# Optimization experiments

Measured on AMD Instinct MI355X. Metric: run time of the kernel, lower is better.

Reference implementation:

```python
import jax, jax.numpy as jnp
import numpy as np

N, P, E, IN = 50000, 4, 500000, 128   # nodes, metapaths, edges/metapath, in_size
H, F = 8, 32                           # num_heads, out_feats per head (hidden_size)
HF = H * F                             # flattened embedding (256)
HS = 128                               # semantic attention hidden size
B, OUT = 128, 2                        # num contracts (graphs), classes
NEG_SLOPE = 0.2                        # DGL GATConv LeakyReLU slope


def setup_inputs() -> dict:
    key = jax.random.key(0)
    ks = jax.random.split(key, 14)
    return {
        "h": jax.random.normal(ks[0], (N, IN), jnp.float32),
        "Wg": jax.random.normal(ks[1], (P, IN, HF), jnp.float32) * 0.1,
        "attn_l": jax.random.normal(ks[2], (P, H, F), jnp.float32) * 0.1,
        "attn_r": jax.random.normal(ks[3], (P, H, F), jnp.float32) * 0.1,
        "gat_bias": jax.random.normal(ks[4], (P, HF), jnp.float32) * 0.1,
        "sem_W1": jax.random.normal(ks[5], (HF, HS), jnp.float32) * 0.1,
        "sem_b1": jax.random.normal(ks[6], (HS,), jnp.float32) * 0.1,
        "sem_W2": jax.random.normal(ks[7], (HS, 1), jnp.float32) * 0.1,
        "cls_W": jax.random.normal(ks[8], (HF, OUT), jnp.float32) * 0.1,
        "cls_b": jax.random.normal(ks[9], (OUT,), jnp.float32) * 0.1,
        "src": jax.random.randint(ks[10], (P, E), 0, N, jnp.int32),
        "dst": jax.random.randint(ks[11], (P, E), 0, N, jnp.int32),
        "graph_ids": jax.random.randint(ks[12], (N,), 0, B, jnp.int32),
    }


def _gat(h, W, al, ar, bias, s, d):
    """One DGL-style GATConv over an edge list (dropout=identity, eval mode)."""
    n = h.shape[0]
    hp = (h @ W).reshape(n, H, F)                 # [N,H,F] projected features
    el = (hp * al).sum(-1)                        # [N,H] src attention term
    er = (hp * ar).sum(-1)                        # [N,H] dst attention term
    e = jax.nn.leaky_relu(el[s] + er[d], NEG_SLOPE)        # [E,H] edge scores
    m = jax.ops.segment_max(e, d, num_segments=n)          # per-dst max (softmax stab.)
    a = jnp.exp(e - m[d])                                  # [E,H]
    den = jax.ops.segment_sum(a, d, num_segments=n)        # [N,H]
    alpha = a / den[d]                                     # edge softmax over in-neighbors
    out = jax.ops.segment_sum(alpha[:, :, None] * hp[s], d, num_segments=n)  # [N,H,F]
    return jax.nn.elu(out + bias.reshape(1, H, F)).reshape(n, HF)


def reference(h, Wg, attn_l, attn_r, gat_bias, sem_W1, sem_b1, sem_W2,
              cls_W, cls_b, src, dst, graph_ids):
    n = h.shape[0]
    # GATConv per meta-path (small fixed loop over P=4 metapaths)
    embs = [_gat(h, Wg[p], attn_l[p], attn_r[p], gat_bias[p], src[p], dst[p])
            for p in range(Wg.shape[0])]
    z = jnp.stack(embs, axis=1)                   # [N,P,HF]
    # Semantic attention over meta-paths
    w = jnp.tanh(z @ sem_W1 + sem_b1) @ sem_W2    # [N,P,1]
    beta = jax.nn.softmax(w.mean(0), axis=0)      # [P,1]
    fused = (beta[None] * z).sum(1)               # [N,HF]
    # Per-graph (filename) mean pooling
    seg = jax.ops.segment_sum(fused, graph_ids, num_segments=B)
    cnt = jax.ops.segment_sum(jnp.ones((n,), fused.dtype), graph_ids, num_segments=B)
    pooled = seg / jnp.maximum(cnt, 1.0)[:, None]  # [B,HF]
    logits = pooled @ cls_W + cls_b                # [B,OUT]
    return (logits, pooled)
```

## Files before the change

### kernel.cpp

```cpp
#include <hip/hip_runtime.h>

#define NN 50000
#define PM 4
#define EE 500000
#define INF_ 128
#define NH 8
#define FF 32
#define HF 256
#define HS 128
#define BG 128
#define OUTC 2

#define NB2 98
#define BCAP 6144
#define BCH 4096
#define NBB 123
#define NGB 13
#define GCAP 576
#define NBG1 782
#define NBE 196
#define NBG2 782

typedef __attribute__((ext_vector_type(8))) short bf16x8;
typedef __attribute__((ext_vector_type(4))) float f32x4;

__device__ __forceinline__ float b2f(unsigned short x) {
  unsigned u = ((unsigned)x) << 16;
  return __builtin_bit_cast(float, u);
}
__device__ __forceinline__ unsigned short f2b(float f) {
  unsigned u = __builtin_bit_cast(unsigned, f);
  u += 0x7fff + ((u >> 16) & 1);
  return (unsigned short)(u >> 16);
}
__device__ __forceinline__ float fexp(float x) { return __expf(x); }
__device__ __forceinline__ float ftanh(float x) {
  float t = __expf(-2.f * fabsf(x));
  float r = (1.f - t) / (1.f + t);
  return copysignf(r, x);
}

__global__ __launch_bounds__(256) void prep_kernel(
    const float* __restrict__ h, const float* __restrict__ Wg,
    const float* __restrict__ W1, const float* __restrict__ al,
    const float* __restrict__ ar,
    unsigned short* __restrict__ h_b, unsigned short* __restrict__ Wb_t,
    unsigned short* __restrict__ W1_t, float* __restrict__ wl,
    float* __restrict__ wr, int* __restrict__ gcnt, int* __restrict__ gcnt2) {
  int b = blockIdx.x;
  int tid = threadIdx.x;
  if (b < 1) {
    for (int i = tid; i < PM * NB2; i += 256) gcnt[i] = 0;
    if (tid < BG) gcnt2[tid] = 0;
    return;
  }
  b -= 1;
  if (b < 6250) {
    int t = b * 256 + tid;
    float4 v = *(const float4*)(h + (size_t)t * 4);
    ushort4 o;
    o.x = f2b(v.x); o.y = f2b(v.y); o.z = f2b(v.z); o.w = f2b(v.w);
    *(ushort4*)(h_b + (size_t)t * 4) = o;
    return;
  }
  b -= 6250;
  if (b < 512) {
    int t = b * 256 + tid;
    int p = t >> 15, rem = t & 32767;
    int n = rem >> 7, k = rem & 127;
    Wb_t[(size_t)p * 32768 + n * 128 + k] = f2b(Wg[(size_t)p * 32768 + k * 256 + n]);
    return;
  }
  b -= 512;
  if (b < 128) {
    int t = b * 256 + tid;
    int n = t >> 8, k = t & 255;
    W1_t[n * 256 + k] = f2b(W1[k * 128 + n]);
    return;
  }
  b -= 128;
  {
    int t = b * 256 + tid;
    int p = t >> 10, rem = t & 1023;
    int k = rem >> 3, hh = rem & 7;
    const float* wrow = Wg + (size_t)p * 32768 + k * 256 + hh * 32;
    const float* alp = al + p * 256 + hh * 32;
    const float* arp = ar + p * 256 + hh * 32;
    float sl = 0.f, sr = 0.f;
    #pragma unroll
    for (int f = 0; f < 32; f++) { sl += wrow[f] * alp[f]; sr += wrow[f] * arp[f]; }
    wl[t] = sl; wr[t] = sr;
  }
}

__global__ __launch_bounds__(256) void bg_kernel(
    const int* __restrict__ src, const int* __restrict__ dst,
    unsigned* __restrict__ bdata, int* __restrict__ gcnt,
    const int* __restrict__ gid, int* __restrict__ glist,
    int* __restrict__ gcnt2) {
  __shared__ __align__(16) char smem[18432];
  int b = blockIdx.x;
  int tid = threadIdx.x;
  if (b < NBB * PM) {
    unsigned* ed = (unsigned*)smem;
    int* hist  = (int*)(smem + BCH * 4);
    int* gbase = hist + NB2;
    int* cur   = gbase + NB2;
    int p = b / NBB, blk = b % NBB;
    int e0 = blk * BCH;
    int n = min(BCH, EE - e0);
    if (tid < NB2) hist[tid] = 0;
    __syncthreads();
    const int* sp = src + (size_t)p * EE + e0;
    const int* dp = dst + (size_t)p * EE + e0;
    for (int i = tid; i < n; i += 256) {
      int s = sp[i], d = dp[i];
      ed[i] = ((unsigned)d << 16) | (unsigned)s;
      atomicAdd(&hist[d >> 9], 1);
    }
    __syncthreads();
    if (tid < NB2) {
      gbase[tid] = atomicAdd(&gcnt[p * NB2 + tid], hist[tid]);
      cur[tid] = 0;
    }
    __syncthreads();
    for (int i = tid; i < n; i += 256) {
      unsigned pk = ed[i];
      int bk = pk >> 25;
      int slot = gbase[bk] + atomicAdd(&cur[bk], 1);
      if (slot < BCAP)
        bdata[((size_t)(p * NB2 + bk)) * BCAP + slot] = pk;
    }
  } else {
    int* gl    = (int*)smem;
    int* hist  = (int*)(smem + BCH * 4);
    int* gbase = hist + BG;
    int* cur   = gbase + BG;
    int blk = b - NBB * PM;
    int e0 = blk * BCH;
    int n = min(BCH, NN - e0);
    if (tid < BG) hist[tid] = 0;
    __syncthreads();
    for (int i = tid; i < n; i += 256) {
      int g = gid[e0 + i];
      gl[i] = g;
      atomicAdd(&hist[g], 1);
    }
    __syncthreads();
    if (tid < BG) {
      gbase[tid] = atomicAdd(&gcnt2[tid], hist[tid]);
      cur[tid] = 0;
    }
    __syncthreads();
    for (int i = tid; i < n; i += 256) {
      int g = gl[i];
      int slot = gbase[g] + atomicAdd(&cur[g], 1);
      if (slot < GCAP) glist[g * GCAP + slot] = e0 + i;
    }
  }
}

__global__ __launch_bounds__(256) void csrify_kernel(
    const unsigned* __restrict__ bdata, const int* __restrict__ gcnt,
    int* __restrict__ off, unsigned short* __restrict__ csr) {
  __shared__ unsigned ebuf[BCAP];
  __shared__ int gc[NB2];
  __shared__ int degc[512];
  __shared__ int loff[513];
  __shared__ int tmp[256];
  __shared__ int base_s;
  int b = blockIdx.x, p = blockIdx.y;
  int tid = threadIdx.x;
  if (tid < NB2) gc[tid] = min(gcnt[p * NB2 + tid], BCAP);
  __syncthreads();
  if (tid == 0) {
    int s = 0;
    for (int i = 0; i < b; i++) s += gc[i];
    base_s = s;
  }
  int cnt = gc[b];
  const unsigned* bp = bdata + ((size_t)(p * NB2 + b)) * BCAP;
  for (int i = tid; i < cnt; i += 256) ebuf[i] = bp[i];
  degc[tid] = 0; degc[256 + tid] = 0;
  __syncthreads();
  for (int i = tid; i < cnt; i += 256)
    atomicAdd(&degc[(ebuf[i] >> 16) & 511], 1);
  __syncthreads();
  int d0 = degc[2 * tid], d1 = degc[2 * tid + 1];
  tmp[tid] = d0 + d1;
  __syncthreads();
  for (int o = 1; o < 256; o <<= 1) {
    int v = (tid >= o) ? tmp[tid - o] : 0;
    __syncthreads();
    tmp[tid] += v;
    __syncthreads();
  }
  int bse = tmp[tid] - d0 - d1;
  loff[2 * tid] = bse; loff[2 * tid + 1] = bse + d0;
  if (tid == 255) loff[512] = tmp[255];
  __syncthreads();
  int base = base_s;
  for (int dl = tid; dl < 512; dl += 256) {
    int n = b * 512 + dl;
    if (n <= NN) off[(size_t)p * (NN + 1) + n] = base + loff[dl];
  }
  degc[tid] = 0; degc[256 + tid] = 0;
  __syncthreads();
  for (int i = tid; i < cnt; i += 256) {
    unsigned pk = ebuf[i];
    int dl = (pk >> 16) & 511;
    int slot = loff[dl] + atomicAdd(&degc[dl], 1);
    csr[(size_t)p * EE + base + slot] = (unsigned short)(pk & 0xffff);
  }
}

__global__ __launch_bounds__(256) void g1elr_kernel(
    const unsigned short* __restrict__ hA, const unsigned short* __restrict__ Bt,
    unsigned short* __restrict__ Cb, const float* __restrict__ wl,
    const float* __restrict__ wr, float* __restrict__ el, float* __restrict__ er,
    int M, int p0, int npaths, size_t cstride, size_t estride) {
  __shared__ __align__(16) char smem[49152];
  int b = blockIdx.x;
  int tid = threadIdx.x;
  int nb1 = NBG1 * 2;
  if (b < nb1) {
    unsigned short* As = (unsigned short*)smem;
    unsigned short* Bs = (unsigned short*)(smem + 16384);
    int row0 = (b >> 1) * 64, col0 = (b & 1) * 128;
    #pragma unroll
    for (int i = 0; i < 4; i++) {
      int c = i * 256 + tid;
      int row = c >> 4, g = c & 15;
      int grow = row0 + row;
      uint4 v = make_uint4(0, 0, 0, 0);
      if (grow < M) v = *(const uint4*)(hA + (size_t)grow * 128 + g * 8);
      *(uint4*)&As[row * 128 + ((g ^ (row & 15)) << 3)] = v;
    }
    int wave = tid >> 6, lane = tid & 63;
    int ln = lane & 15, quad = lane >> 4;
    int mbase = (wave >> 1) * 32, nbase = (wave & 1) * 64;
    bf16x8 afr[4][2];
    bool afr_ok = false;
    for (int pl = 0; pl < npaths; pl++) {
      const unsigned short* Bp = Bt + (size_t)(p0 + pl) * 32768;
      #pragma unroll
      for (int i = 0; i < 8; i++) {
        int c = i * 256 + tid;
        int row = c >> 4, g = c & 15;
        uint4 v = *(const uint4*)(Bp + (size_t)(col0 + row) * 128 + g * 8);
        *(uint4*)&Bs[row * 128 + ((g ^ (row & 15)) << 3)] = v;
      }
      __syncthreads();
      if (!afr_ok) {
        #pragma unroll
        for (int ks = 0; ks < 4; ks++) {
          int g = ks * 4 + quad;
          #pragma unroll
          for (int mi = 0; mi < 2; mi++) {
            int r = mbase + mi * 16 + ln;
            afr[ks][mi] = *(const bf16x8*)&As[r * 128 + ((g ^ ln) << 3)];
          }
        }
        afr_ok = true;
      }
      f32x4 acc[2][4] = {};
      #pragma unroll
      for (int ks = 0; ks < 4; ks++) {
        int g = ks * 4 + quad;
        bf16x8 bb[4];
        #pragma unroll
        for (int ni = 0; ni < 4; ni++) {
          int r = nbase + ni * 16 + ln;
          bb[ni] = *(const bf16x8*)&Bs[r * 128 + ((g ^ ln) << 3)];
        }
        #pragma unroll
        for (int mi = 0; mi < 2; mi++)
          #pragma unroll
          for (int ni = 0; ni < 4; ni++)
            acc[mi][ni] = __builtin_amdgcn_mfma_f32_16x16x32_bf16(afr[ks][mi], bb[ni], acc[mi][ni], 0, 0, 0);
      }
      unsigned short* Cp = Cb + (size_t)pl * cstride;
      #pragma unroll
      for (int mi = 0; mi < 2; mi++) {
        int gm0 = row0 + mbase + mi * 16 + quad * 4;
        #pragma unroll
        for (int ni = 0; ni < 4; ni++) {
          int gn = col0 + nbase + ni * 16 + ln;
          #pragma unroll
          for (int r = 0; r < 4; r++) {
            int gm = gm0 + r;
            if (gm < M) Cp[(size_t)gm * 256 + gn] = f2b(acc[mi][ni][r]);
          }
        }
      }
      __syncthreads();
    }
  } else {
    float* wls = (float*)smem;
    float* wrs = wls + 1024;
    int t = b - nb1;
    int pl = t / NBE, nblk = t % NBE;
    const float* wlp = wl + (size_t)(p0 + pl) * 1024;
    const float* wrp = wr + (size_t)(p0 + pl) * 1024;
    float* elp = el + (size_t)pl * estride;
    float* erp = er + (size_t)pl * estride;
    for (int i = tid; i < 1024; i += 256) { wls[i] = wlp[i]; wrs[i] = wrp[i]; }
    __syncthreads();
    int n = nblk * 256 + tid;
    if (n >= M) return;
    float accl[8] = {}, accr[8] = {};
    for (int kk = 0; kk < 16; kk++) {
      uint4 raw = *(const uint4*)(hA + (size_t)n * 128 + kk * 8);
      unsigned uu[4] = {raw.x, raw.y, raw.z, raw.w};
      #pragma unroll
      for (int q = 0; q < 4; q++) {
        float v0 = __builtin_bit_cast(float, uu[q] << 16);
        float v1 = __builtin_bit_cast(float, uu[q] & 0xffff0000u);
        int k = kk * 8 + q * 2;
        #pragma unroll
        for (int hh = 0; hh < 8; hh++) {
          accl[hh] += v0 * wls[k * 8 + hh] + v1 * wls[(k + 1) * 8 + hh];
          accr[hh] += v0 * wrs[k * 8 + hh] + v1 * wrs[(k + 1) * 8 + hh];
        }
      }
    }
    *(float4*)(elp + (size_t)n * 8)     = make_float4(accl[0], accl[1], accl[2], accl[3]);
    *(float4*)(elp + (size_t)n * 8 + 4) = make_float4(accl[4], accl[5], accl[6], accl[7]);
    *(float4*)(erp + (size_t)n * 8)     = make_float4(accr[0], accr[1], accr[2], accr[3]);
    *(float4*)(erp + (size_t)n * 8 + 4) = make_float4(accr[4], accr[5], accr[6], accr[7]);
  }
}

__global__ __launch_bounds__(256) void agg_kernel(
    const unsigned short* __restrict__ hp_b, const float* __restrict__ el,
    const float* __restrict__ er, const unsigned short* __restrict__ csr,
    const int* __restrict__ off, const float* __restrict__ bias,
    unsigned short* __restrict__ emb_b, int N, int p0,
    size_t hstride, size_t estride, size_t embstride) {
  int pl = blockIdx.y;
  int p = p0 + pl;
  const unsigned short* hp = hp_b + (size_t)pl * hstride;
  const float* elp = el + (size_t)pl * estride;
  const float* erp = er + (size_t)pl * estride;
  const unsigned short* csrp = csr + (size_t)p * EE;
  const int* offp = off + (size_t)p * (NN + 1);
  const float* bp = bias + (size_t)p * HF;
  unsigned short* embp = emb_b + (size_t)pl * embstride;
  int n = blockIdx.x * 4 + (threadIdx.x >> 6);
  if (n >= N) return;
  int lane = threadIdx.x & 63;
  int h = lane >> 3;
  int e0 = offp[n], e1 = offp[n + 1];
  float erh = erp[n * NH + h];
  float den = 0.f, a0 = 0.f, a1 = 0.f, a2 = 0.f, a3 = 0.f;
  int e = e0;
  for (; e + 8 <= e1; e += 8) {
    int s[8];
    #pragma unroll
    for (int j = 0; j < 8; j++) s[j] = csrp[e + j];
    float x[8];
    #pragma unroll
    for (int j = 0; j < 8; j++) x[j] = elp[s[j] * NH + h];
    ushort4 hv[8];
    #pragma unroll
    for (int j = 0; j < 8; j++)
      hv[j] = *(const ushort4*)(hp + (size_t)s[j] * HF + lane * 4);
    float w[8];
    #pragma unroll
    for (int j = 0; j < 8; j++) {
      float xx = x[j] + erh;
      xx = fmaxf(xx, 0.2f * xx);
      w[j] = fexp(xx);
    }
    den += ((w[0] + w[1]) + (w[2] + w[3])) + ((w[4] + w[5]) + (w[6] + w[7]));
    a0 += ((w[0] * b2f(hv[0].x) + w[1] * b2f(hv[1].x)) + (w[2] * b2f(hv[2].x) + w[3] * b2f(hv[3].x)))
        + ((w[4] * b2f(hv[4].x) + w[5] * b2f(hv[5].x)) + (w[6] * b2f(hv[6].x) + w[7] * b2f(hv[7].x)));
    a1 += ((w[0] * b2f(hv[0].y) + w[1] * b2f(hv[1].y)) + (w[2] * b2f(hv[2].y) + w[3] * b2f(hv[3].y)))
        + ((w[4] * b2f(hv[4].y) + w[5] * b2f(hv[5].y)) + (w[6] * b2f(hv[6].y) + w[7] * b2f(hv[7].y)));
    a2 += ((w[0] * b2f(hv[0].z) + w[1] * b2f(hv[1].z)) + (w[2] * b2f(hv[2].z) + w[3] * b2f(hv[3].z)))
        + ((w[4] * b2f(hv[4].z) + w[5] * b2f(hv[5].z)) + (w[6] * b2f(hv[6].z) + w[7] * b2f(hv[7].z)));
    a3 += ((w[0] * b2f(hv[0].w) + w[1] * b2f(hv[1].w)) + (w[2] * b2f(hv[2].w) + w[3] * b2f(hv[3].w)))
        + ((w[4] * b2f(hv[4].w) + w[5] * b2f(hv[5].w)) + (w[6] * b2f(hv[6].w) + w[7] * b2f(hv[7].w)));
  }
  if (e + 4 <= e1) {
    int s0 = csrp[e], s1 = csrp[e + 1], s2 = csrp[e + 2], s3 = csrp[e + 3];
    float x0 = elp[s0 * NH + h] + erh;
    float x1 = elp[s1 * NH + h] + erh;
    float x2 = elp[s2 * NH + h] + erh;
    float x3 = elp[s3 * NH + h] + erh;
    ushort4 h0 = *(const ushort4*)(hp + (size_t)s0 * HF + lane * 4);
    ushort4 h1 = *(const ushort4*)(hp + (size_t)s1 * HF + lane * 4);
    ushort4 h2 = *(const ushort4*)(hp + (size_t)s2 * HF + lane * 4);
    ushort4 h3 = *(const ushort4*)(hp + (size_t)s3 * HF + lane * 4);
    x0 = fmaxf(x0, 0.2f * x0); x1 = fmaxf(x1, 0.2f * x1);
    x2 = fmaxf(x2, 0.2f * x2); x3 = fmaxf(x3, 0.2f * x3);
    float w0 = fexp(x0), w1 = fexp(x1), w2 = fexp(x2), w3 = fexp(x3);
    den += (w0 + w1) + (w2 + w3);
    a0 += (w0 * b2f(h0.x) + w1 * b2f(h1.x)) + (w2 * b2f(h2.x) + w3 * b2f(h3.x));
    a1 += (w0 * b2f(h0.y) + w1 * b2f(h1.y)) + (w2 * b2f(h2.y) + w3 * b2f(h3.y));
    a2 += (w0 * b2f(h0.z) + w1 * b2f(h1.z)) + (w2 * b2f(h2.z) + w3 * b2f(h3.z));
    a3 += (w0 * b2f(h0.w) + w1 * b2f(h1.w)) + (w2 * b2f(h2.w) + w3 * b2f(h3.w));
    e += 4;
  }
  for (; e < e1; e++) {
    int s = csrp[e];
    float x = elp[s * NH + h] + erh;
    x = fmaxf(x, 0.2f * x);
    float w = fexp(x);
    den += w;
    ushort4 hv = *(const ushort4*)(hp + (size_t)s * HF + lane * 4);
    a0 += w * b2f(hv.x); a1 += w * b2f(hv.y);
    a2 += w * b2f(hv.z); a3 += w * b2f(hv.w);
  }
  float inv = (den > 0.f) ? 1.f / den : 0.f;
  float4 bv = *(const float4*)(bp + lane * 4);
  float o0 = a0 * inv + bv.x, o1 = a1 * inv + bv.y;
  float o2 = a2 * inv + bv.z, o3 = a3 * inv + bv.w;
  o0 = (o0 > 0.f) ? o0 : fexp(o0) - 1.f;
  o1 = (o1 > 0.f) ? o1 : fexp(o1) - 1.f;
  o2 = (o2 > 0.f) ? o2 : fexp(o2) - 1.f;
  o3 = (o3 > 0.f) ? o3 : fexp(o3) - 1.f;
  ushort4 ov;
  ov.x = f2b(o0); ov.y = f2b(o1); ov.z = f2b(o2); ov.w = f2b(o3);
  *(ushort4*)(embp + (size_t)n * HF + lane * 4) = ov;
}

__global__ __launch_bounds__(256) void g2pool_kernel(
    const unsigned short* __restrict__ A, const unsigned short* __restrict__ Bt,
    const float* __restrict__ b1, const float* __restrict__ W2,
    float* __restrict__ wpart, const int* __restrict__ glist,
    const int* __restrict__ gcnt2, float* __restrict__ pool,
    int M, int p0, int npaths, size_t astride) {
  __shared__ __align__(16) char smem[49168];
  int b = blockIdx.x;
  int tid = threadIdx.x;
  int nb2 = NBG2 * npaths;
  if (b < nb2) {
    unsigned short* As = (unsigned short*)smem;
    unsigned short* Bs = (unsigned short*)(smem + 16384);
    float* wred = (float*)(smem + 49152);
    int bx = b % NBG2, pl = b / NBG2;
    const unsigned short* Ap = A + (size_t)pl * astride;
    int row0 = bx * 64;
    int wave = tid >> 6, lane = tid & 63;
    int ln = lane & 15, quad = lane >> 4;
    int mbase = (wave >> 1) * 32, nbase = (wave & 1) * 64;
    f32x4 acc[2][4] = {};
    for (int kc = 0; kc < 2; kc++) {
      #pragma unroll
      for (int i = 0; i < 4; i++) {
        int c = i * 256 + tid;
        int row = c >> 4, g = c & 15;
        int grow = row0 + row;
        uint4 v = make_uint4(0, 0, 0, 0);
        if (grow < M) v = *(const uint4*)(Ap + (size_t)grow * 256 + kc * 128 + g * 8);
        *(uint4*)&As[row * 128 + ((g ^ (row & 15)) << 3)] = v;
      }
      #pragma unroll
      for (int i = 0; i < 8; i++) {
        int c = i * 256 + tid;
        int row = c >> 4, g = c & 15;
        uint4 v = *(const uint4*)(Bt + (size_t)row * 256 + kc * 128 + g * 8);
        *(uint4*)&Bs[row * 128 + ((g ^ (row & 15)) << 3)] = v;
      }
      __syncthreads();
      #pragma unroll
      for (int ks = 0; ks < 4; ks++) {
        int g = ks * 4 + quad;
        bf16x8 a[2], bb[4];
        #pragma unroll
        for (int mi = 0; mi < 2; mi++) {
          int r = mbase + mi * 16 + ln;
          a[mi] = *(const bf16x8*)&As[r * 128 + ((g ^ ln) << 3)];
        }
        #pragma unroll
        for (int ni = 0; ni < 4; ni++) {
          int r = nbase + ni * 16 + ln;
          bb[ni] = *(const bf16x8*)&Bs[r * 128 + ((g ^ ln) << 3)];
        }
        #pragma unroll
        for (int mi = 0; mi < 2; mi++)
          #pragma unroll
          for (int ni = 0; ni < 4; ni++)
            acc[mi][ni] = __builtin_amdgcn_mfma_f32_16x16x32_bf16(a[mi], bb[ni], acc[mi][ni], 0, 0, 0);
      }
      __syncthreads();
    }
    float b1v[4], w2v[4];
    #pragma unroll
    for (int ni = 0; ni < 4; ni++) {
      int col = nbase + ni * 16 + ln;
      b1v[ni] = b1[col]; w2v[ni] = W2[col];
    }
    float s = 0.f;
    #pragma unroll
    for (int mi = 0; mi < 2; mi++) {
      int gm0 = row0 + mbase + mi * 16 + quad * 4;
      #pragma unroll
      for (int r = 0; r < 4; r++) {
        if (gm0 + r < M) {
          #pragma unroll
          for (int ni = 0; ni < 4; ni++)
            s += ftanh(acc[mi][ni][r] + b1v[ni]) * w2v[ni];
        }
      }
    }
    #pragma unroll
    for (int o = 32; o > 0; o >>= 1) s += __shfl_down(s, o);
    if (lane == 0) wred[wave] = s;
    __syncthreads();
    if (tid == 0)
      wpart[(size_t)(p0 + pl) * NBG2 + bx] =
          (wred[0] + wred[1]) + (wred[2] + wred[3]);
  } else {
    int* nl = (int*)smem;
    float* sm = (float*)(smem + GCAP * 4);
    int i0 = b - nb2;
    int g = i0 % BG, pl = i0 / BG;
    const unsigned short* embp = A + (size_t)pl * astride;
    int cnt = min(gcnt2[g], GCAP);
    for (int i = tid; i < cnt; i += 256) nl[i] = glist[g * GCAP + i];
    __syncthreads();
    int sub = tid >> 6, lane = tid & 63;
    float a0 = 0.f, a1 = 0.f, a2 = 0.f, a3 = 0.f;
    for (int i = sub; i < cnt; i += 4) {
      ushort4 v = *(const ushort4*)(embp + (size_t)nl[i] * HF + lane * 4);
      a0 += b2f(v.x); a1 += b2f(v.y); a2 += b2f(v.z); a3 += b2f(v.w);
    }
    sm[(sub * 64 + lane) * 4 + 0] = a0;
    sm[(sub * 64 + lane) * 4 + 1] = a1;
    sm[(sub * 64 + lane) * 4 + 2] = a2;
    sm[(sub * 64 + lane) * 4 + 3] = a3;
    __syncthreads();
    int fl = tid >> 2, j = tid & 3;
    float s = sm[(0 * 64 + fl) * 4 + j] + sm[(1 * 64 + fl) * 4 + j]
            + sm[(2 * 64 + fl) * 4 + j] + sm[(3 * 64 + fl) * 4 + j];
    pool[((size_t)(p0 + pl) * BG + g) * HF + tid] = s;
  }
}

__global__ __launch_bounds__(256) void final_kernel(
    const float* __restrict__ pool, const float* __restrict__ wpart,
    const int* __restrict__ gcnt2, const float* __restrict__ clsW,
    const float* __restrict__ clsb, float* __restrict__ out, int N) {
  int b = blockIdx.x;
  int f = threadIdx.x;
  __shared__ float red[256];
  float wm[PM];
  #pragma unroll
  for (int p = 0; p < PM; p++) {
    float s = 0.f;
    for (int i = f; i < NBG2; i += 256) s += wpart[(size_t)p * NBG2 + i];
    red[f] = s;
    __syncthreads();
    for (int st = 128; st > 0; st >>= 1) {
      if (f < st) red[f] += red[f + st];
      __syncthreads();
    }
    wm[p] = red[0] / (float)N;
    __syncthreads();
  }
  float c = fmaxf((float)gcnt2[b], 1.f);
  float mx = -1e30f;
  #pragma unroll
  for (int p = 0; p < PM; p++) mx = fmaxf(mx, wm[p]);
  float es = 0.f, e[PM];
  #pragma unroll
  for (int p = 0; p < PM; p++) { e[p] = expf(wm[p] - mx); es += e[p]; }
  float v = 0.f;
  #pragma unroll
  for (int p = 0; p < PM; p++)
    v += (e[p] / es) * pool[((size_t)p * BG + b) * HF + f];
  v /= c;
  out[256 + (size_t)b * HF + f] = v;
  __shared__ float sm[256];
  sm[f] = v * clsW[f * 2 + 0];
  __syncthreads();
  for (int st = 128; st > 0; st >>= 1) {
    if (f < st) sm[f] += sm[f + st];
    __syncthreads();
  }
  float l0 = sm[0];
  __syncthreads();
  sm[f] = v * clsW[f * 2 + 1];
  __syncthreads();
  for (int st = 128; st > 0; st >>= 1) {
    if (f < st) sm[f] += sm[f + st];
    __syncthreads();
  }
  if (f == 0) {
    out[b * 2 + 0] = l0 + clsb[0];
    out[b * 2 + 1] = sm[0] + clsb[1];
  }
}

extern "C" void kernel_launch(void* const* d_in, const int* in_sizes, int n_in,
                              void* d_out, int out_size, void* d_ws, size_t ws_size,
                              hipStream_t stream) {
  const float* h      = (const float*)d_in[0];
  const float* Wg     = (const float*)d_in[1];
  const float* attn_l = (const float*)d_in[2];
  const float* attn_r = (const float*)d_in[3];
  const float* gatb   = (const float*)d_in[4];
  const float* semW1  = (const float*)d_in[5];
  const float* semb1  = (const float*)d_in[6];
  const float* semW2  = (const float*)d_in[7];
  const float* clsW   = (const float*)d_in[8];
  const float* clsb   = (const float*)d_in[9];
  const int*   src    = (const int*)d_in[10];
  const int*   dst    = (const int*)d_in[11];
  const int*   gid    = (const int*)d_in[12];
  float* out = (float*)d_out;

  auto layout_size = [](int PMg) -> size_t {
    size_t o = 0;
    auto alloc = [&](size_t bytes) { o += (bytes + 255) & ~(size_t)255; };
    alloc((size_t)NN * INF_ * 2);
    alloc((size_t)PMg * NN * HF * 2);
    alloc((size_t)PMg * NN * HF * 2);
    alloc((size_t)PM * HF * INF_ * 2);
    alloc((size_t)HS * HF * 2);
    alloc((size_t)PM * INF_ * NH * 4);
    alloc((size_t)PM * INF_ * NH * 4);
    alloc((size_t)PMg * NN * NH * 4);
    alloc((size_t)PMg * NN * NH * 4);
    alloc((size_t)PM * NB2 * BCAP * 4);
    alloc((size_t)PM * NB2 * 4);
    alloc((size_t)BG * GCAP * 4);
    alloc((size_t)BG * 4);
    alloc((size_t)PM * (NN + 1) * 4);
    alloc((size_t)PM * EE * 2);
    alloc((size_t)PM * BG * HF * 4);
    alloc((size_t)PM * NBG2 * 4);
    return o;
  };
  int PMg = (layout_size(4) <= ws_size) ? 4 : 1;

  char* ws = (char*)d_ws;
  size_t o = 0;
  auto alloc = [&](size_t bytes) { size_t r = o; o += (bytes + 255) & ~(size_t)255; return r; };
  unsigned short* h_b   = (unsigned short*)(ws + alloc((size_t)NN * INF_ * 2));
  unsigned short* hp_b  = (unsigned short*)(ws + alloc((size_t)PMg * NN * HF * 2));
  unsigned short* emb_b = (unsigned short*)(ws + alloc((size_t)PMg * NN * HF * 2));
  unsigned short* Wb_t  = (unsigned short*)(ws + alloc((size_t)PM * HF * INF_ * 2));
  unsigned short* W1_t  = (unsigned short*)(ws + alloc((size_t)HS * HF * 2));
  float* wl    = (float*)(ws + alloc((size_t)PM * INF_ * NH * 4));
  float* wr    = (float*)(ws + alloc((size_t)PM * INF_ * NH * 4));
  float* el    = (float*)(ws + alloc((size_t)PMg * NN * NH * 4));
  float* er    = (float*)(ws + alloc((size_t)PMg * NN * NH * 4));
  unsigned* bdata = (unsigned*)(ws + alloc((size_t)PM * NB2 * BCAP * 4));
  int*   gcnt  = (int*)(ws + alloc((size_t)PM * NB2 * 4));
  int*   glist = (int*)(ws + alloc((size_t)BG * GCAP * 4));
  int*   gcnt2 = (int*)(ws + alloc((size_t)BG * 4));
  int*   off   = (int*)(ws + alloc((size_t)PM * (NN + 1) * 4));
  unsigned short* csr = (unsigned short*)(ws + alloc((size_t)PM * EE * 2));
  float* pool  = (float*)(ws + alloc((size_t)PM * BG * HF * 4));
  float* wpart = (float*)(ws + alloc((size_t)PM * NBG2 * 4));

  const size_t hpS  = (PMg == 4) ? (size_t)NN * HF : 0;
  const size_t embS = hpS;
  const size_t elS  = (PMg == 4) ? (size_t)NN * NH : 0;

  prep_kernel<<<1 + 6250 + 512 + 128 + 16, 256, 0, stream>>>(
      h, Wg, semW1, attn_l, attn_r, h_b, Wb_t, W1_t, wl, wr, gcnt, gcnt2);
  bg_kernel<<<NBB * PM + NGB, 256, 0, stream>>>(src, dst, bdata, gcnt, gid, glist, gcnt2);
  csrify_kernel<<<dim3(NB2, PM), 256, 0, stream>>>(bdata, gcnt, off, csr);

  if (PMg == 4) {
    g1elr_kernel<<<NBG1 * 2 + NBE * 4, 256, 0, stream>>>(
        h_b, Wb_t, hp_b, wl, wr, el, er, NN, 0, 4, hpS, elS);
    agg_kernel<<<dim3((NN + 3) / 4, 4), 256, 0, stream>>>(
        hp_b, el, er, csr, off, gatb, emb_b, NN, 0, hpS, elS, embS);
    g2pool_kernel<<<NBG2 * 4 + BG * 4, 256, 0, stream>>>(
        emb_b, W1_t, semb1, semW2, wpart, glist, gcnt2, pool, NN, 0, 4, embS);
  } else {
    for (int p = 0; p < PM; p++) {
      g1elr_kernel<<<NBG1 * 2 + NBE, 256, 0, stream>>>(
          h_b, Wb_t, hp_b, wl, wr, el, er, NN, p, 1, 0, 0);
      agg_kernel<<<dim3((NN + 3) / 4, 1), 256, 0, stream>>>(
          hp_b, el, er, csr, off, gatb, emb_b, NN, p, 0, 0, 0);
      g2pool_kernel<<<NBG2 + BG, 256, 0, stream>>>(
          emb_b, W1_t, semb1, semW2, wpart, glist, gcnt2, pool, NN, p, 1, 0);
    }
  }

  final_kernel<<<BG, 256, 0, stream>>>(pool, wpart, gcnt2, clsW, clsb, out, NN);
}
```

Measured before the change: 432.3 us.

## Merge CSR build into GEMM kernel and stage GEMM output through LDS

The CSR construction blocks move into the same launch as the projection GEMM and el/er blocks, so the two independent stages can run concurrently and one kernel launch goes away. Separately, the GEMM epilogue now writes bf16 results into a padded LDS tile and then stores full rows with 16-byte vector writes, replacing scattered 2-byte global stores. This costs extra barriers and LDS traffic per path, and the fused kernel's shared-memory footprint is set by the larger of the two roles.

```diff
diff --git a/kernel.cpp b/kernel.cpp
--- a/kernel.cpp
+++ b/kernel.cpp
@@ -20,6 +20,7 @@
 #define NBG1 782
 #define NBE 196
 #define NBG2 782
+#define CTS 136
 
 typedef __attribute__((ext_vector_type(8))) short bf16x8;
 typedef __attribute__((ext_vector_type(4))) float f32x4;
@@ -160,72 +161,73 @@
   }
 }
 
-__global__ __launch_bounds__(256) void csrify_kernel(
+__global__ __launch_bounds__(256) void cg1_kernel(
     const unsigned* __restrict__ bdata, const int* __restrict__ gcnt,
-    int* __restrict__ off, unsigned short* __restrict__ csr) {
-  __shared__ unsigned ebuf[BCAP];
-  __shared__ int gc[NB2];
-  __shared__ int degc[512];
-  __shared__ int loff[513];
-  __shared__ int tmp[256];
-  __shared__ int base_s;
-  int b = blockIdx.x, p = blockIdx.y;
-  int tid = threadIdx.x;
-  if (tid < NB2) gc[tid] = min(gcnt[p * NB2 + tid], BCAP);
-  __syncthreads();
-  if (tid == 0) {
-    int s = 0;
-    for (int i = 0; i < b; i++) s += gc[i];
-    base_s = s;
-  }
-  int cnt = gc[b];
-  const unsigned* bp = bdata + ((size_t)(p * NB2 + b)) * BCAP;
-  for (int i = tid; i < cnt; i += 256) ebuf[i] = bp[i];
-  degc[tid] = 0; degc[256 + tid] = 0;
-  __syncthreads();
-  for (int i = tid; i < cnt; i += 256)
-    atomicAdd(&degc[(ebuf[i] >> 16) & 511], 1);
-  __syncthreads();
-  int d0 = degc[2 * tid], d1 = degc[2 * tid + 1];
-  tmp[tid] = d0 + d1;
-  __syncthreads();
-  for (int o = 1; o < 256; o <<= 1) {
-    int v = (tid >= o) ? tmp[tid - o] : 0;
-    __syncthreads();
-    tmp[tid] += v;
-    __syncthreads();
-  }
-  int bse = tmp[tid] - d0 - d1;
-  loff[2 * tid] = bse; loff[2 * tid + 1] = bse + d0;
-  if (tid == 255) loff[512] = tmp[255];
-  __syncthreads();
-  int base = base_s;
-  for (int dl = tid; dl < 512; dl += 256) {
-    int n = b * 512 + dl;
-    if (n <= NN) off[(size_t)p * (NN + 1) + n] = base + loff[dl];
-  }
-  degc[tid] = 0; degc[256 + tid] = 0;
-  __syncthreads();
-  for (int i = tid; i < cnt; i += 256) {
-    unsigned pk = ebuf[i];
-    int dl = (pk >> 16) & 511;
-    int slot = loff[dl] + atomicAdd(&degc[dl], 1);
-    csr[(size_t)p * EE + base + slot] = (unsigned short)(pk & 0xffff);
-  }
-}
-
-__global__ __launch_bounds__(256) void g1elr_kernel(
+    int* __restrict__ off, unsigned short* __restrict__ csr,
     const unsigned short* __restrict__ hA, const unsigned short* __restrict__ Bt,
     unsigned short* __restrict__ Cb, const float* __restrict__ wl,
     const float* __restrict__ wr, float* __restrict__ el, float* __restrict__ er,
-    int M, int p0, int npaths, size_t cstride, size_t estride) {
+    int M, int p0, int npaths, int ncsr, size_t cstride, size_t estride) {
   __shared__ __align__(16) char smem[49152];
   int b = blockIdx.x;
   int tid = threadIdx.x;
+  if (b < ncsr) {
+    unsigned* ebuf = (unsigned*)smem;
+    int* gc    = (int*)(smem + 24576);
+    int* degc  = (int*)(smem + 24968);
+    int* loff  = (int*)(smem + 27016);
+    int* tmp   = (int*)(smem + 29068);
+    int* base_p = (int*)(smem + 30092);
+    int bb = b % NB2, p = b / NB2;
+    if (tid < NB2) gc[tid] = min(gcnt[p * NB2 + tid], BCAP);
+    __syncthreads();
+    if (tid == 0) {
+      int s = 0;
+      for (int i = 0; i < bb; i++) s += gc[i];
+      *base_p = s;
+    }
+    int cnt = gc[bb];
+    const unsigned* bp = bdata + ((size_t)(p * NB2 + bb)) * BCAP;
+    for (int i = tid; i < cnt; i += 256) ebuf[i] = bp[i];
+    degc[tid] = 0; degc[256 + tid] = 0;
+    __syncthreads();
+    for (int i = tid; i < cnt; i += 256)
+      atomicAdd(&degc[(ebuf[i] >> 16) & 511], 1);
+    __syncthreads();
+    int d0 = degc[2 * tid], d1 = degc[2 * tid + 1];
+    tmp[tid] = d0 + d1;
+    __syncthreads();
+    for (int o = 1; o < 256; o <<= 1) {
+      int v = (tid >= o) ? tmp[tid - o] : 0;
+      __syncthreads();
+      tmp[tid] += v;
+      __syncthreads();
+    }
+    int bse = tmp[tid] - d0 - d1;
+    loff[2 * tid] = bse; loff[2 * tid + 1] = bse + d0;
+    if (tid == 255) loff[512] = tmp[255];
+    __syncthreads();
+    int base = *base_p;
+    for (int dl = tid; dl < 512; dl += 256) {
+      int n = bb * 512 + dl;
+      if (n <= NN) off[(size_t)p * (NN + 1) + n] = base + loff[dl];
+    }
+    degc[tid] = 0; degc[256 + tid] = 0;
+    __syncthreads();
+    for (int i = tid; i < cnt; i += 256) {
+      unsigned pk = ebuf[i];
+      int dl = (pk >> 16) & 511;
+      int slot = loff[dl] + atomicAdd(&degc[dl], 1);
+      csr[(size_t)p * EE + base + slot] = (unsigned short)(pk & 0xffff);
+    }
+    return;
+  }
+  b -= ncsr;
   int nb1 = NBG1 * 2;
   if (b < nb1) {
     unsigned short* As = (unsigned short*)smem;
     unsigned short* Bs = (unsigned short*)(smem + 16384);
+    unsigned short* Ct = (unsigned short*)smem;
     int row0 = (b >> 1) * 64, col0 = (b & 1) * 128;
     #pragma unroll
     for (int i = 0; i < 4; i++) {
@@ -279,18 +281,28 @@
           for (int ni = 0; ni < 4; ni++)
             acc[mi][ni] = __builtin_amdgcn_mfma_f32_16x16x32_bf16(afr[ks][mi], bb[ni], acc[mi][ni], 0, 0, 0);
       }
-      unsigned short* Cp = Cb + (size_t)pl * cstride;
+      __syncthreads();
       #pragma unroll
       for (int mi = 0; mi < 2; mi++) {
-        int gm0 = row0 + mbase + mi * 16 + quad * 4;
+        int lr0 = mbase + mi * 16 + quad * 4;
         #pragma unroll
         for (int ni = 0; ni < 4; ni++) {
-          int gn = col0 + nbase + ni * 16 + ln;
+          int lc = nbase + ni * 16 + ln;
           #pragma unroll
-          for (int r = 0; r < 4; r++) {
-            int gm = gm0 + r;
-            if (gm < M) Cp[(size_t)gm * 256 + gn] = f2b(acc[mi][ni][r]);
-          }
+          for (int r = 0; r < 4; r++)
+            Ct[(lr0 + r) * CTS + lc] = f2b(acc[mi][ni][r]);
+        }
+      }
+      __syncthreads();
+      unsigned short* Cp = Cb + (size_t)pl * cstride;
+      int r2 = tid >> 2, seg = tid & 3;
+      int gm = row0 + r2;
+      if (gm < M) {
+        #pragma unroll
+        for (int k = 0; k < 4; k++) {
+          int c = seg * 8 + k * 32;
+          uint4 v = *(const uint4*)&Ct[r2 * CTS + c];
+          *(uint4*)(Cp + (size_t)gm * 256 + col0 + c) = v;
         }
       }
       __syncthreads();
@@ -664,19 +676,23 @@
   prep_kernel<<<1 + 6250 + 512 + 128 + 16, 256, 0, stream>>>(
       h, Wg, semW1, attn_l, attn_r, h_b, Wb_t, W1_t, wl, wr, gcnt, gcnt2);
   bg_kernel<<<NBB * PM + NGB, 256, 0, stream>>>(src, dst, bdata, gcnt, gid, glist, gcnt2);
-  csrify_kernel<<<dim3(NB2, PM), 256, 0, stream>>>(bdata, gcnt, off, csr);
 
   if (PMg == 4) {
-    g1elr_kernel<<<NBG1 * 2 + NBE * 4, 256, 0, stream>>>(
-        h_b, Wb_t, hp_b, wl, wr, el, er, NN, 0, 4, hpS, elS);
+    cg1_kernel<<<NB2 * PM + NBG1 * 2 + NBE * 4, 256, 0, stream>>>(
+        bdata, gcnt, off, csr, h_b, Wb_t, hp_b, wl, wr, el, er,
+        NN, 0, 4, NB2 * PM, hpS, elS);
     agg_kernel<<<dim3((NN + 3) / 4, 4), 256, 0, stream>>>(
         hp_b, el, er, csr, off, gatb, emb_b, NN, 0, hpS, elS, embS);
     g2pool_kernel<<<NBG2 * 4 + BG * 4, 256, 0, stream>>>(
         emb_b, W1_t, semb1, semW2, wpart, glist, gcnt2, pool, NN, 0, 4, embS);
   } else {
+    cg1_kernel<<<NB2 * PM, 256, 0, stream>>>(
+        bdata, gcnt, off, csr, h_b, Wb_t, hp_b, wl, wr, el, er,
+        NN, 0, 0, NB2 * PM, 0, 0);
     for (int p = 0; p < PM; p++) {
-      g1elr_kernel<<<NBG1 * 2 + NBE, 256, 0, stream>>>(
-          h_b, Wb_t, hp_b, wl, wr, el, er, NN, p, 1, 0, 0);
+      cg1_kernel<<<NBG1 * 2 + NBE, 256, 0, stream>>>(
+          bdata, gcnt, off, csr, h_b, Wb_t, hp_b, wl, wr, el, er,
+          NN, p, 1, 0, 0, 0);
       agg_kernel<<<dim3((NN + 3) / 4, 1), 256, 0, stream>>>(
           hp_b, el, er, csr, off, gatb, emb_b, NN, p, 0, 0, 0);
       g2pool_kernel<<<NBG2 + BG, 256, 0, stream>>>(
```

After: 420.7 us. 2.7% less time.
